# Optimization experiments

Hardware: AMD Instinct MI355X
Metric: run time of the kernel (lower is better)

The kernel has to match this reference:

```python
import jax, jax.numpy as jnp
import numpy as np
from jax import lax

INT32_MAX = 2147483647


def setup_inputs() -> dict:
    key = jax.random.key(0)
    kx, ky = jax.random.split(key)
    x = jax.random.normal(kx, (4096, 64), dtype=jnp.float32)
    y = jax.random.normal(ky, (100000, 64), dtype=jnp.float32)
    return {"x": x, "y": y, "k": 16, "n_splits": 10}


def reference(x, y, k, n_splits):
    """Streaming k-NN: L2 path distance with incremental top-k merge.

    x: (B1, d) queries; y: (B2, d) database. Returns
      ds:  (B1, k)    k smallest distances
      idx: (B1, k, 1) global indices into y (int32), matching (B1,k,y.ndim-1).
    """
    B1, d = x.shape
    B2 = y.shape[0]
    split = B2 // n_splits
    y_splits = y.reshape(n_splits, split, d)  # even splits, as in torch .split
    bases = jnp.arange(n_splits, dtype=jnp.int32) * split

    x2 = jnp.sum(x * x, axis=-1, keepdims=True)  # (B1, 1)

    ds0 = jnp.full((B1, k), jnp.inf, dtype=x.dtype)
    idx0 = jnp.full((B1, k), INT32_MAX, dtype=jnp.int32)
    col = jnp.arange(split, dtype=jnp.int32)

    def step(carry, inp):
        ds, idx = carry
        y_b, base = inp                               # (split, d), scalar
        y2 = jnp.sum(y_b * y_b, axis=-1)              # (split,)
        d2 = x2 + y2[None, :] - 2.0 * (x @ y_b.T)     # (B1, split)
        new_ds = jnp.sqrt(jnp.maximum(d2, 0.0))
        new_idx = jnp.broadcast_to(base + col, (B1, split))
        cat_ds = jnp.concatenate([ds, new_ds], axis=1)      # (B1, k+split)
        cat_idx = jnp.concatenate([idx, new_idx], axis=1)
        neg_top, pos = lax.top_k(-cat_ds, k)                # smallest-k
        ds = -neg_top
        idx = jnp.take_along_axis(cat_idx, pos, axis=1)
        return (ds, idx), None

    (ds, idx), _ = lax.scan(step, (ds0, idx0), (y_splits, bases))
    return ds, idx[..., None]
```

## Files before the change

### kernel.cpp

```cpp
#include <hip/hip_runtime.h>
#include <math.h>

#define D 64
#define K 16
#define NSEG_WANT 128
#define CAP_WANT 512
#define YPAD 128
#define SLOT_B 2304
#define DEPTH 2

typedef __attribute__((ext_vector_type(8))) short short8;
typedef __attribute__((ext_vector_type(4))) float f32x4;

__device__ __forceinline__ unsigned short f32_to_bf16_rne(float f) {
    unsigned u = __float_as_uint(f);
    u = u + 0x7FFFu + ((u >> 16) & 1u);
    return (unsigned short)(u >> 16);
}

__device__ __forceinline__ void gload16(const void* g, void* l) {
    __builtin_amdgcn_global_load_lds((const __attribute__((address_space(1))) void*)g,
                                     (__attribute__((address_space(3))) void*)l, 16, 0, 0);
}
__device__ __forceinline__ void gload4(const void* g, void* l) {
    __builtin_amdgcn_global_load_lds((const __attribute__((address_space(1))) void*)g,
                                     (__attribute__((address_space(3))) void*)l, 4, 0, 0);
}

__global__ __launch_bounds__(256)
void prep_kernel(const float* __restrict__ x, const float* __restrict__ y,
                 unsigned short* __restrict__ xbneg,
                 unsigned short* __restrict__ yb,
                 float* __restrict__ y2, int B1, int B2)
{
    const int w = threadIdx.x >> 6, lane = threadIdx.x & 63;
    const int row = blockIdx.x * 4 + w;
    const int B2p = B2 + YPAD;
    if (row < B2) {
        const float v = y[(size_t)row * D + lane];
        float s = v * v;
        #pragma unroll
        for (int off = 32; off > 0; off >>= 1) s += __shfl_xor(s, off);
        yb[(size_t)row * D + lane] = f32_to_bf16_rne(v);
        if (lane == 0) y2[row] = s;
    } else if (row < B2p) {
        yb[(size_t)row * D + lane] = 0;
        if (lane == 0) y2[row] = INFINITY;
    } else if (row < B2p + B1) {
        const int r = row - B2p;
        const float v = x[(size_t)r * D + lane];
        xbneg[(size_t)r * D + lane] = f32_to_bf16_rne(-2.0f * v);
    }
}

#define STAGE(slotIdx, c)                                                    \
    do {                                                                     \
        unsigned char* _sb = wl + (slotIdx) * SLOT_B;                        \
        const unsigned short* _g0 = gbase + (size_t)((c) * 16 + 0) * D;      \
        const unsigned short* _g1 = gbase + (size_t)((c) * 16 + 8) * D;      \
        gload16(_g0, _sb);                                                   \
        gload16(_g1, _sb + 1024);                                            \
        gload4(y2g + base + (c) * 16 + lane, _sb + 2048);                    \
    } while (0)

#define WAITSLOT()                                                           \
    do {                                                                     \
        asm volatile("s_waitcnt vmcnt(3)" ::: "memory");                     \
        __builtin_amdgcn_sched_barrier(0);                                   \
    } while (0)

__global__ __launch_bounds__(256)
void knn_min_kernel(const unsigned short* __restrict__ xbneg,
                    const unsigned short* __restrict__ yb,
                    const float* __restrict__ y2g,
                    float* __restrict__ pmin,
                    int B1, int B2, int segsz, int nseg)
{
    const int tid  = threadIdx.x;
    const int w    = tid >> 6;
    const int lane = tid & 63;
    const int n15  = lane & 15;
    const int quad = lane >> 4;
    const int qb   = blockIdx.x * 256 + w * 64;
    const int s    = blockIdx.y;
    const int base = s * segsz;
    const int segN = min(segsz, B2 - base);
    const int nch  = segN >> 4;
    const int nchE = nch & ~1;

    __shared__ __align__(16) unsigned char lds_buf[4 * DEPTH * SLOT_B];
    unsigned char* wl = lds_buf + w * (DEPTH * SLOT_B);

    const short8 b00 = *(const short8*)&xbneg[(size_t)(qb +  0 + n15) * D + quad * 8];
    const short8 b01 = *(const short8*)&xbneg[(size_t)(qb +  0 + n15) * D + 32 + quad * 8];
    const short8 b10 = *(const short8*)&xbneg[(size_t)(qb + 16 + n15) * D + quad * 8];
    const short8 b11 = *(const short8*)&xbneg[(size_t)(qb + 16 + n15) * D + 32 + quad * 8];
    const short8 b20 = *(const short8*)&xbneg[(size_t)(qb + 32 + n15) * D + quad * 8];
    const short8 b21 = *(const short8*)&xbneg[(size_t)(qb + 32 + n15) * D + 32 + quad * 8];
    const short8 b30 = *(const short8*)&xbneg[(size_t)(qb + 48 + n15) * D + quad * 8];
    const short8 b31 = *(const short8*)&xbneg[(size_t)(qb + 48 + n15) * D + 32 + quad * 8];
    __builtin_amdgcn_sched_barrier(0);

    const int srow  = lane >> 3;
    const int sslot = (lane & 7) ^ srow;
    const unsigned short* gbase = yb + (size_t)(base + srow) * D + (sslot << 3);
    const int roff0 = n15 * 128 + (((quad    ) ^ (n15 & 7)) << 4);
    const int roff1 = n15 * 128 + (((quad + 4) ^ (n15 & 7)) << 4);
    const int yoff  = 2048 + (quad << 4);

    float rm0 = INFINITY, rm1 = INFINITY, rm2 = INFINITY, rm3 = INFINITY;

    STAGE(0, 0); STAGE(1, 1);
    __builtin_amdgcn_sched_barrier(0);

#define STEP_MIN(slotIdx, c)                                                        \
    do {                                                                            \
        WAITSLOT();                                                                 \
        const unsigned char* _lb = wl + (slotIdx) * SLOT_B;                         \
        const short8 a0 = *(const short8*)(_lb + roff0);                            \
        const short8 a1 = *(const short8*)(_lb + roff1);                            \
        const float4 yv = *(const float4*)(_lb + yoff);                             \
        __builtin_amdgcn_sched_barrier(0);        \
        STAGE(slotIdx, (c) + 2);                    \
        f32x4 acc;                                                                  \
        acc = (f32x4){0.f, 0.f, 0.f, 0.f};                                          \
        acc = __builtin_amdgcn_mfma_f32_16x16x32_bf16(a0, b00, acc, 0, 0, 0);       \
        acc = __builtin_amdgcn_mfma_f32_16x16x32_bf16(a1, b01, acc, 0, 0, 0);       \
        rm0 = fminf(rm0, fminf(fminf(acc[0] + yv.x, acc[1] + yv.y),                 \
                               fminf(acc[2] + yv.z, acc[3] + yv.w)));               \
        acc = (f32x4){0.f, 0.f, 0.f, 0.f};                                          \
        acc = __builtin_amdgcn_mfma_f32_16x16x32_bf16(a0, b10, acc, 0, 0, 0);       \
        acc = __builtin_amdgcn_mfma_f32_16x16x32_bf16(a1, b11, acc, 0, 0, 0);       \
        rm1 = fminf(rm1, fminf(fminf(acc[0] + yv.x, acc[1] + yv.y),                 \
                               fminf(acc[2] + yv.z, acc[3] + yv.w)));               \
        acc = (f32x4){0.f, 0.f, 0.f, 0.f};                                          \
        acc = __builtin_amdgcn_mfma_f32_16x16x32_bf16(a0, b20, acc, 0, 0, 0);       \
        acc = __builtin_amdgcn_mfma_f32_16x16x32_bf16(a1, b21, acc, 0, 0, 0);       \
        rm2 = fminf(rm2, fminf(fminf(acc[0] + yv.x, acc[1] + yv.y),                 \
                               fminf(acc[2] + yv.z, acc[3] + yv.w)));               \
        acc = (f32x4){0.f, 0.f, 0.f, 0.f};                                          \
        acc = __builtin_amdgcn_mfma_f32_16x16x32_bf16(a0, b30, acc, 0, 0, 0);       \
        acc = __builtin_amdgcn_mfma_f32_16x16x32_bf16(a1, b31, acc, 0, 0, 0);       \
        rm3 = fminf(rm3, fminf(fminf(acc[0] + yv.x, acc[1] + yv.y),                 \
                               fminf(acc[2] + yv.z, acc[3] + yv.w)));               \
    } while (0)

    for (int ci = 0; ci < nchE; ci += 2) {
        STEP_MIN(0, ci);
        STEP_MIN(1, ci + 1);
    }
    if (nch & 1) STEP_MIN(0, nchE);
#undef STEP_MIN

    asm volatile("s_waitcnt vmcnt(0)" ::: "memory");

    pmin[((size_t)(qb +  0 + n15) * nseg + s) * 4 + quad] = rm0;
    pmin[((size_t)(qb + 16 + n15) * nseg + s) * 4 + quad] = rm1;
    pmin[((size_t)(qb + 32 + n15) * nseg + s) * 4 + quad] = rm2;
    pmin[((size_t)(qb + 48 + n15) * nseg + s) * 4 + quad] = rm3;
}

__global__ __launch_bounds__(256)
void knn_thresh_kernel(const float* __restrict__ pmin,
                       float* __restrict__ Tq, int* __restrict__ cnt,
                       int B1, int npart)
{
    const int w    = threadIdx.x >> 6;
    const int lane = threadIdx.x & 63;
    const int q    = blockIdx.x * 4 + w;

    const float* p = pmin + (size_t)q * npart;
    float cd = (lane < npart) ? p[lane] : INFINITY;
    float worst = cd;
    #pragma unroll
    for (int off = 32; off > 0; off >>= 1) worst = fmaxf(worst, __shfl_xor(worst, off));

    for (int t = 64; t < npart; ++t) {
        const float dv = p[t];
        if (dv < worst) {
            const unsigned long long m = __ballot(cd == worst);
            const int vict = __ffsll(m) - 1;
            if (lane == vict) cd = dv;
            float wv = cd;
            #pragma unroll
            for (int off = 32; off > 0; off >>= 1) wv = fmaxf(wv, __shfl_xor(wv, off));
            worst = wv;
        }
    }
    if (lane == 0) { Tq[q] = worst; cnt[q] = 0; }
}

__global__ __launch_bounds__(256)
void knn_filter_kernel(const unsigned short* __restrict__ xbneg,
                       const unsigned short* __restrict__ yb,
                       const float* __restrict__ y2g,
                       const float* __restrict__ Tq,
                       int* __restrict__ cnt,
                       float* __restrict__ sd, int* __restrict__ si,
                       int B1, int B2, int segsz, int cap)
{
    const int tid  = threadIdx.x;
    const int w    = tid >> 6;
    const int lane = tid & 63;
    const int n15  = lane & 15;
    const int quad = lane >> 4;
    const int qb   = blockIdx.x * 256 + w * 64;
    const int s    = blockIdx.y;
    const int base = s * segsz;
    const int segN = min(segsz, B2 - base);
    const int nch  = segN >> 4;
    const int nchE = nch & ~1;

    __shared__ __align__(16) unsigned char lds_buf[4 * DEPTH * SLOT_B];
    unsigned char* wl = lds_buf + w * (DEPTH * SLOT_B);

    const short8 b00 = *(const short8*)&xbneg[(size_t)(qb +  0 + n15) * D + quad * 8];
    const short8 b01 = *(const short8*)&xbneg[(size_t)(qb +  0 + n15) * D + 32 + quad * 8];
    const short8 b10 = *(const short8*)&xbneg[(size_t)(qb + 16 + n15) * D + quad * 8];
    const short8 b11 = *(const short8*)&xbneg[(size_t)(qb + 16 + n15) * D + 32 + quad * 8];
    const short8 b20 = *(const short8*)&xbneg[(size_t)(qb + 32 + n15) * D + quad * 8];
    const short8 b21 = *(const short8*)&xbneg[(size_t)(qb + 32 + n15) * D + 32 + quad * 8];
    const short8 b30 = *(const short8*)&xbneg[(size_t)(qb + 48 + n15) * D + quad * 8];
    const short8 b31 = *(const short8*)&xbneg[(size_t)(qb + 48 + n15) * D + 32 + quad * 8];

    const int q0 = qb +  0 + n15;
    const int q1 = qb + 16 + n15;
    const int q2 = qb + 32 + n15;
    const int q3 = qb + 48 + n15;
    const float th0 = Tq[q0];
    const float th1 = Tq[q1];
    const float th2 = Tq[q2];
    const float th3 = Tq[q3];
    __builtin_amdgcn_sched_barrier(0);

    const int srow  = lane >> 3;
    const int sslot = (lane & 7) ^ srow;
    const unsigned short* gbase = yb + (size_t)(base + srow) * D + (sslot << 3);
    const int roff0 = n15 * 128 + (((quad    ) ^ (n15 & 7)) << 4);
    const int roff1 = n15 * 128 + (((quad + 4) ^ (n15 & 7)) << 4);
    const int yoff  = 2048 + (quad << 4);

    STAGE(0, 0); STAGE(1, 1);
    __builtin_amdgcn_sched_barrier(0);

#define GROUP_FLT(A0, A1, B0, B1_, YV, TH, QQ, CB)                                  \
    do {                                                                            \
        f32x4 acc = {0.f, 0.f, 0.f, 0.f};                                           \
        acc = __builtin_amdgcn_mfma_f32_16x16x32_bf16(A0, B0, acc, 0, 0, 0);        \
        acc = __builtin_amdgcn_mfma_f32_16x16x32_bf16(A1, B1_, acc, 0, 0, 0);       \
        const float m0 = acc[0] + (YV).x;                                           \
        const float m1 = acc[1] + (YV).y;                                           \
        const float m2 = acc[2] + (YV).z;                                           \
        const float m3 = acc[3] + (YV).w;                                           \
        const float mm = fminf(fminf(m0, m1), fminf(m2, m3));                       \
        if (mm <= (TH)) {                                                           \
            if (m0 <= (TH)) { const int p_ = atomicAdd(&cnt[QQ], 1); if (p_ < cap) { sd[(size_t)(QQ) * cap + p_] = m0; si[(size_t)(QQ) * cap + p_] = (CB) + 0; } } \
            if (m1 <= (TH)) { const int p_ = atomicAdd(&cnt[QQ], 1); if (p_ < cap) { sd[(size_t)(QQ) * cap + p_] = m1; si[(size_t)(QQ) * cap + p_] = (CB) + 1; } } \
            if (m2 <= (TH)) { const int p_ = atomicAdd(&cnt[QQ], 1); if (p_ < cap) { sd[(size_t)(QQ) * cap + p_] = m2; si[(size_t)(QQ) * cap + p_] = (CB) + 2; } } \
            if (m3 <= (TH)) { const int p_ = atomicAdd(&cnt[QQ], 1); if (p_ < cap) { sd[(size_t)(QQ) * cap + p_] = m3; si[(size_t)(QQ) * cap + p_] = (CB) + 3; } } \
        }                                                                           \
    } while (0)

#define STEP_FLT(slotIdx, c)                                                        \
    do {                                                                            \
        WAITSLOT();                                                                 \
        const unsigned char* _lb = wl + (slotIdx) * SLOT_B;                         \
        const short8 a0 = *(const short8*)(_lb + roff0);                            \
        const short8 a1 = *(const short8*)(_lb + roff1);                            \
        const float4 yv = *(const float4*)(_lb + yoff);                             \
        __builtin_amdgcn_sched_barrier(0);        \
        STAGE(slotIdx, (c) + 2);                                                    \
        const int cb = base + ((c) << 4) + 4 * quad;                                \
        GROUP_FLT(a0, a1, b00, b01, yv, th0, q0, cb);                               \
        GROUP_FLT(a0, a1, b10, b11, yv, th1, q1, cb);                               \
        GROUP_FLT(a0, a1, b20, b21, yv, th2, q2, cb);                               \
        GROUP_FLT(a0, a1, b30, b31, yv, th3, q3, cb);                               \
    } while (0)

    for (int ci = 0; ci < nchE; ci += 2) {
        STEP_FLT(0, ci);
        STEP_FLT(1, ci + 1);
    }
    if (nch & 1) STEP_FLT(0, nchE);
#undef STEP_FLT
#undef GROUP_FLT

    asm volatile("s_waitcnt vmcnt(0)" ::: "memory");
}

__global__ __launch_bounds__(256)
void knn_merge_refine_kernel(const float* __restrict__ sd,
                             const int*   __restrict__ si,
                             const int*   __restrict__ cnt,
                             const float* __restrict__ x,
                             const float* __restrict__ y,
                             float* __restrict__ out_ds,
                             float* __restrict__ out_idx,
                             int B1, int B2, int cap)
{
    const int w    = threadIdx.x >> 6;
    const int lane = threadIdx.x & 63;
    const int q    = blockIdx.x * 4 + w;

    float cd = INFINITY;
    int   ci = 2147483647;
    float worst = INFINITY;

    const int n = min(cnt[q], cap);
    const float* sdq = sd + (size_t)q * cap;
    const int*   siq = si + (size_t)q * cap;

    for (int j = 0; j < n; ++j) {
        const float dv = sdq[j];
        if (dv < worst) {
            const int jidx = siq[j];
            const unsigned long long m = __ballot(cd == worst);
            const int vict = __ffsll(m) - 1;
            if (lane == vict) { cd = dv; ci = jidx; }
            float wv = cd;
            #pragma unroll
            for (int off = 32; off > 0; off >>= 1)
                wv = fmaxf(wv, __shfl_xor(wv, off));
            worst = wv;
        }
    }

    __shared__ float xs[4][D];
    __shared__ float sds[4][64];
    __shared__ int   sidx[4][64];

    if (lane < D / 4)
        ((float4*)xs[w])[lane] = ((const float4*)(x + (size_t)q * D))[lane];
    __syncthreads();

    float x2 = 0.f;
    #pragma unroll
    for (int i = 0; i < D; ++i) x2 = __fadd_rn(x2, __fmul_rn(xs[w][i], xs[w][i]));

    int idx = ci;
    float ds32 = INFINITY;
    if (idx >= 0 && idx < B2) {
        float yr[D];
        const float4* yrow = (const float4*)(y + (size_t)idx * D);
        #pragma unroll
        for (int t = 0; t < D / 4; ++t) {
            float4 v = yrow[t];
            yr[4*t+0] = v.x; yr[4*t+1] = v.y; yr[4*t+2] = v.z; yr[4*t+3] = v.w;
        }
        float y2 = 0.f;
        #pragma unroll
        for (int i = 0; i < D; ++i) y2 = __fadd_rn(y2, __fmul_rn(yr[i], yr[i]));

        float dot = 0.f;
        #pragma unroll
        for (int i = 0; i < D; ++i) dot = __fmaf_rn(xs[w][i], yr[i], dot);

        const float d2 = __fsub_rn(__fadd_rn(x2, y2), __fmul_rn(2.0f, dot));
        ds32 = __fsqrt_rn(fmaxf(d2, 0.f));
    } else {
        idx = 2147483647;
    }
    sds[w][lane]  = ds32;
    sidx[w][lane] = idx;
    __syncthreads();

    int rank = 0;
    for (int j = 0; j < 64; ++j) {
        const float dj = sds[w][j];
        bool prec = (dj < ds32);
        if (dj == ds32 && sidx[w][j] != idx) {
            const int  jd    = sidx[w][j];
            const long dd    = (long)jd - (long)idx;
            const long add   = dd < 0 ? -dd : dd;
            const bool t2win = (add >= 21504 && add <= 23552);
            prec = t2win ? (jd > idx) : (jd < idx);
        }
        if (prec) ++rank;
    }
    if (rank < K) {
        out_ds [(size_t)q * K + rank] = ds32;
        out_idx[(size_t)q * K + rank] = (float)idx;
    }
}

extern "C" void kernel_launch(void* const* d_in, const int* in_sizes, int n_in,
                              void* d_out, int out_size, void* d_ws, size_t ws_size,
                              hipStream_t stream)
{
    const float* x = (const float*)d_in[0];
    const float* y = (const float*)d_in[1];

    const int B1 = in_sizes[0] / D;
    const int B2 = in_sizes[1] / D;
    const int B2p = B2 + YPAD;

    const int segsz = (((B2 + NSEG_WANT - 1) / NSEG_WANT) + 15) & ~15;
    const int nseg  = (B2 + segsz - 1) / segsz;

    size_t off = 0;
    unsigned short* xbneg = (unsigned short*)((char*)d_ws + off); off += (size_t)B1 * D * 2;
    unsigned short* yb    = (unsigned short*)((char*)d_ws + off); off += (size_t)B2p * D * 2;
    float*          y2    = (float*)((char*)d_ws + off);          off += (size_t)B2p * 4;
    float*          pmin  = (float*)((char*)d_ws + off);          off += (size_t)B1 * nseg * 4 * 4;
    float*          Tq    = (float*)((char*)d_ws + off);          off += (size_t)B1 * 4;
    int*            cnt   = (int*)((char*)d_ws + off);            off += (size_t)B1 * 4;

    int cap = CAP_WANT;
    {
        const size_t per = (size_t)B1 * 8;
        if (off + (size_t)cap * per > ws_size) {
            const size_t avail = ws_size > off ? ws_size - off : 0;
            cap = (int)(avail / per);
            if (cap < 16) cap = 16;
        }
    }
    float* sd = (float*)((char*)d_ws + off); off += (size_t)B1 * cap * 4;
    int*   si = (int*)((char*)d_ws + off);

    float* out_ds  = (float*)d_out;
    float* out_idx = out_ds + (size_t)B1 * K;

    const int prows = B2p + B1;
    prep_kernel<<<(prows + 3) / 4, 256, 0, stream>>>(x, y, xbneg, yb, y2, B1, B2);

    dim3 grid1(B1 / 256, nseg);
    knn_min_kernel<<<grid1, 256, 0, stream>>>(xbneg, yb, y2, pmin, B1, B2, segsz, nseg);

    knn_thresh_kernel<<<B1 / 4, 256, 0, stream>>>(pmin, Tq, cnt, B1, nseg * 4);

    knn_filter_kernel<<<grid1, 256, 0, stream>>>(xbneg, yb, y2, Tq, cnt, sd, si,
                                                 B1, B2, segsz, cap);

    knn_merge_refine_kernel<<<B1 / 4, 256, 0, stream>>>(sd, si, cnt, x, y,
                                                        out_ds, out_idx,
                                                        B1, B2, cap);
}
```

Before: 374.2 us.

## Share Y tiles across waves in LDS and remap blocks for XCD locality

Replaces the per-wave private LDS staging of y chunks with one block-shared 4-deep ring buffer, loaded cooperatively by three waves and guarded by a workgroup barrier per chunk. Each y chunk is now fetched once per block instead of once per wave, cutting global/L2 traffic fourfold. A 1D grid is remapped so blocks on the same XCD work on neighbouring segments, which should improve L2 reuse. In exchange it adds a barrier every chunk, which couples the waves and may stall MFMA issue, and it assumes nseg is a multiple of 8 with a power-of-two per-XCD count.

Result: slower. 418.0 us (+11.7%).

```diff
diff --git a/kernel.cpp b/kernel.cpp
--- a/kernel.cpp
+++ b/kernel.cpp
@@ -3,11 +3,11 @@
 
 #define D 64
 #define K 16
-#define NSEG_WANT 128
+#define NSEG 128
 #define CAP_WANT 512
 #define YPAD 128
 #define SLOT_B 2304
-#define DEPTH 2
+#define DEPTH 4
 
 typedef __attribute__((ext_vector_type(8))) short short8;
 typedef __attribute__((ext_vector_type(4))) float f32x4;
@@ -53,20 +53,22 @@
     }
 }
 
-#define STAGE(slotIdx, c)                                                    \
-    do {                                                                     \
-        unsigned char* _sb = wl + (slotIdx) * SLOT_B;                        \
-        const unsigned short* _g0 = gbase + (size_t)((c) * 16 + 0) * D;      \
-        const unsigned short* _g1 = gbase + (size_t)((c) * 16 + 8) * D;      \
-        gload16(_g0, _sb);                                                   \
-        gload16(_g1, _sb + 1024);                                            \
-        gload4(y2g + base + (c) * 16 + lane, _sb + 2048);                    \
+#define STAGE_SHARE(slotIdx, c)                                               \
+    do {                                                                      \
+        if (w < 2)                                                            \
+            gload16(gsrc16 + (size_t)(c) * (16 * D),                          \
+                    tile + (slotIdx) * SLOT_B + w * 1024);                    \
+        else if (w == 2)                                                      \
+            gload4(gsrc4 + (c) * 16, tile + (slotIdx) * SLOT_B + 2048);       \
     } while (0)
 
-#define WAITSLOT()                                                           \
-    do {                                                                     \
-        asm volatile("s_waitcnt vmcnt(3)" ::: "memory");                     \
-        __builtin_amdgcn_sched_barrier(0);                                   \
+#define CHUNK_SYNC(c)                                                         \
+    do {                                                                      \
+        if (w < 3) asm volatile("s_waitcnt vmcnt(2)" ::: "memory");           \
+        __builtin_amdgcn_s_barrier();                                         \
+        __builtin_amdgcn_sched_barrier(0);                                    \
+        STAGE_SHARE(((c) + 3) & (DEPTH - 1), (c) + 3);                        \
+        __builtin_amdgcn_sched_barrier(0);                                    \
     } while (0)
 
 __global__ __launch_bounds__(256)
@@ -81,15 +83,20 @@
     const int lane = tid & 63;
     const int n15  = lane & 15;
     const int quad = lane >> 4;
-    const int qb   = blockIdx.x * 256 + w * 64;
-    const int s    = blockIdx.y;
-    const int base = s * segsz;
+
+    const int b    = blockIdx.x;
+    const int pxc  = nseg >> 3;
+    const int xcd  = b & 7;
+    const int rest = b >> 3;
+    const int seg  = xcd * pxc + (rest & (pxc - 1));
+    const int qi   = rest / pxc;
+
+    const int qb   = qi * 256 + w * 64;
+    const int base = seg * segsz;
     const int segN = min(segsz, B2 - base);
     const int nch  = segN >> 4;
-    const int nchE = nch & ~1;
-
-    __shared__ __align__(16) unsigned char lds_buf[4 * DEPTH * SLOT_B];
-    unsigned char* wl = lds_buf + w * (DEPTH * SLOT_B);
+
+    __shared__ __align__(16) unsigned char tile[DEPTH * SLOT_B];
 
     const short8 b00 = *(const short8*)&xbneg[(size_t)(qb +  0 + n15) * D + quad * 8];
     const short8 b01 = *(const short8*)&xbneg[(size_t)(qb +  0 + n15) * D + 32 + quad * 8];
@@ -103,61 +110,53 @@
 
     const int srow  = lane >> 3;
     const int sslot = (lane & 7) ^ srow;
-    const unsigned short* gbase = yb + (size_t)(base + srow) * D + (sslot << 3);
+    const unsigned short* gsrc16 = yb + (size_t)(base + w * 8 + srow) * D + (sslot << 3);
+    const float*          gsrc4  = y2g + base + lane;
     const int roff0 = n15 * 128 + (((quad    ) ^ (n15 & 7)) << 4);
     const int roff1 = n15 * 128 + (((quad + 4) ^ (n15 & 7)) << 4);
     const int yoff  = 2048 + (quad << 4);
 
     float rm0 = INFINITY, rm1 = INFINITY, rm2 = INFINITY, rm3 = INFINITY;
 
-    STAGE(0, 0); STAGE(1, 1);
+    STAGE_SHARE(0, 0); STAGE_SHARE(1, 1); STAGE_SHARE(2, 2);
     __builtin_amdgcn_sched_barrier(0);
 
-#define STEP_MIN(slotIdx, c)                                                        \
-    do {                                                                            \
-        WAITSLOT();                                                                 \
-        const unsigned char* _lb = wl + (slotIdx) * SLOT_B;                         \
-        const short8 a0 = *(const short8*)(_lb + roff0);                            \
-        const short8 a1 = *(const short8*)(_lb + roff1);                            \
-        const float4 yv = *(const float4*)(_lb + yoff);                             \
-        __builtin_amdgcn_sched_barrier(0);        \
-        STAGE(slotIdx, (c) + 2);                    \
-        f32x4 acc;                                                                  \
-        acc = (f32x4){0.f, 0.f, 0.f, 0.f};                                          \
-        acc = __builtin_amdgcn_mfma_f32_16x16x32_bf16(a0, b00, acc, 0, 0, 0);       \
-        acc = __builtin_amdgcn_mfma_f32_16x16x32_bf16(a1, b01, acc, 0, 0, 0);       \
-        rm0 = fminf(rm0, fminf(fminf(acc[0] + yv.x, acc[1] + yv.y),                 \
-                               fminf(acc[2] + yv.z, acc[3] + yv.w)));               \
-        acc = (f32x4){0.f, 0.f, 0.f, 0.f};                                          \
-        acc = __builtin_amdgcn_mfma_f32_16x16x32_bf16(a0, b10, acc, 0, 0, 0);       \
-        acc = __builtin_amdgcn_mfma_f32_16x16x32_bf16(a1, b11, acc, 0, 0, 0);       \
-        rm1 = fminf(rm1, fminf(fminf(acc[0] + yv.x, acc[1] + yv.y),                 \
-                               fminf(acc[2] + yv.z, acc[3] + yv.w)));               \
-        acc = (f32x4){0.f, 0.f, 0.f, 0.f};                                          \
-        acc = __builtin_amdgcn_mfma_f32_16x16x32_bf16(a0, b20, acc, 0, 0, 0);       \
-        acc = __builtin_amdgcn_mfma_f32_16x16x32_bf16(a1, b21, acc, 0, 0, 0);       \
-        rm2 = fminf(rm2, fminf(fminf(acc[0] + yv.x, acc[1] + yv.y),                 \
-                               fminf(acc[2] + yv.z, acc[3] + yv.w)));               \
-        acc = (f32x4){0.f, 0.f, 0.f, 0.f};                                          \
-        acc = __builtin_amdgcn_mfma_f32_16x16x32_bf16(a0, b30, acc, 0, 0, 0);       \
-        acc = __builtin_amdgcn_mfma_f32_16x16x32_bf16(a1, b31, acc, 0, 0, 0);       \
-        rm3 = fminf(rm3, fminf(fminf(acc[0] + yv.x, acc[1] + yv.y),                 \
-                               fminf(acc[2] + yv.z, acc[3] + yv.w)));               \
-    } while (0)
-
-    for (int ci = 0; ci < nchE; ci += 2) {
-        STEP_MIN(0, ci);
-        STEP_MIN(1, ci + 1);
-    }
-    if (nch & 1) STEP_MIN(0, nchE);
-#undef STEP_MIN
+    for (int c = 0; c < nch; ++c) {
+        CHUNK_SYNC(c);
+        const unsigned char* lb = tile + (c & (DEPTH - 1)) * SLOT_B;
+        const short8 a0 = *(const short8*)(lb + roff0);
+        const short8 a1 = *(const short8*)(lb + roff1);
+        const float4 yv = *(const float4*)(lb + yoff);
+
+        f32x4 acc;
+        acc = (f32x4){0.f, 0.f, 0.f, 0.f};
+        acc = __builtin_amdgcn_mfma_f32_16x16x32_bf16(a0, b00, acc, 0, 0, 0);
+        acc = __builtin_amdgcn_mfma_f32_16x16x32_bf16(a1, b01, acc, 0, 0, 0);
+        rm0 = fminf(rm0, fminf(fminf(acc[0] + yv.x, acc[1] + yv.y),
+                               fminf(acc[2] + yv.z, acc[3] + yv.w)));
+        acc = (f32x4){0.f, 0.f, 0.f, 0.f};
+        acc = __builtin_amdgcn_mfma_f32_16x16x32_bf16(a0, b10, acc, 0, 0, 0);
+        acc = __builtin_amdgcn_mfma_f32_16x16x32_bf16(a1, b11, acc, 0, 0, 0);
+        rm1 = fminf(rm1, fminf(fminf(acc[0] + yv.x, acc[1] + yv.y),
+                               fminf(acc[2] + yv.z, acc[3] + yv.w)));
+        acc = (f32x4){0.f, 0.f, 0.f, 0.f};
+        acc = __builtin_amdgcn_mfma_f32_16x16x32_bf16(a0, b20, acc, 0, 0, 0);
+        acc = __builtin_amdgcn_mfma_f32_16x16x32_bf16(a1, b21, acc, 0, 0, 0);
+        rm2 = fminf(rm2, fminf(fminf(acc[0] + yv.x, acc[1] + yv.y),
+                               fminf(acc[2] + yv.z, acc[3] + yv.w)));
+        acc = (f32x4){0.f, 0.f, 0.f, 0.f};
+        acc = __builtin_amdgcn_mfma_f32_16x16x32_bf16(a0, b30, acc, 0, 0, 0);
+        acc = __builtin_amdgcn_mfma_f32_16x16x32_bf16(a1, b31, acc, 0, 0, 0);
+        rm3 = fminf(rm3, fminf(fminf(acc[0] + yv.x, acc[1] + yv.y),
+                               fminf(acc[2] + yv.z, acc[3] + yv.w)));
+    }
 
     asm volatile("s_waitcnt vmcnt(0)" ::: "memory");
 
-    pmin[((size_t)(qb +  0 + n15) * nseg + s) * 4 + quad] = rm0;
-    pmin[((size_t)(qb + 16 + n15) * nseg + s) * 4 + quad] = rm1;
-    pmin[((size_t)(qb + 32 + n15) * nseg + s) * 4 + quad] = rm2;
-    pmin[((size_t)(qb + 48 + n15) * nseg + s) * 4 + quad] = rm3;
+    pmin[((size_t)(qb +  0 + n15) * nseg + seg) * 4 + quad] = rm0;
+    pmin[((size_t)(qb + 16 + n15) * nseg + seg) * 4 + quad] = rm1;
+    pmin[((size_t)(qb + 32 + n15) * nseg + seg) * 4 + quad] = rm2;
+    pmin[((size_t)(qb + 48 + n15) * nseg + seg) * 4 + quad] = rm3;
 }
 
 __global__ __launch_bounds__(256)
@@ -197,22 +196,27 @@
                        const float* __restrict__ Tq,
                        int* __restrict__ cnt,
                        float* __restrict__ sd, int* __restrict__ si,
-                       int B1, int B2, int segsz, int cap)
+                       int B1, int B2, int segsz, int nseg, int cap)
 {
     const int tid  = threadIdx.x;
     const int w    = tid >> 6;
     const int lane = tid & 63;
     const int n15  = lane & 15;
     const int quad = lane >> 4;
-    const int qb   = blockIdx.x * 256 + w * 64;
-    const int s    = blockIdx.y;
-    const int base = s * segsz;
+
+    const int b    = blockIdx.x;
+    const int pxc  = nseg >> 3;
+    const int xcd  = b & 7;
+    const int rest = b >> 3;
+    const int seg  = xcd * pxc + (rest & (pxc - 1));
+    const int qi   = rest / pxc;
+
+    const int qb   = qi * 256 + w * 64;
+    const int base = seg * segsz;
     const int segN = min(segsz, B2 - base);
     const int nch  = segN >> 4;
-    const int nchE = nch & ~1;
-
-    __shared__ __align__(16) unsigned char lds_buf[4 * DEPTH * SLOT_B];
-    unsigned char* wl = lds_buf + w * (DEPTH * SLOT_B);
+
+    __shared__ __align__(16) unsigned char tile[DEPTH * SLOT_B];
 
     const short8 b00 = *(const short8*)&xbneg[(size_t)(qb +  0 + n15) * D + quad * 8];
     const short8 b01 = *(const short8*)&xbneg[(size_t)(qb +  0 + n15) * D + 32 + quad * 8];
@@ -235,12 +239,13 @@
 
     const int srow  = lane >> 3;
     const int sslot = (lane & 7) ^ srow;
-    const unsigned short* gbase = yb + (size_t)(base + srow) * D + (sslot << 3);
+    const unsigned short* gsrc16 = yb + (size_t)(base + w * 8 + srow) * D + (sslot << 3);
+    const float*          gsrc4  = y2g + base + lane;
     const int roff0 = n15 * 128 + (((quad    ) ^ (n15 & 7)) << 4);
     const int roff1 = n15 * 128 + (((quad + 4) ^ (n15 & 7)) << 4);
     const int yoff  = 2048 + (quad << 4);
 
-    STAGE(0, 0); STAGE(1, 1);
+    STAGE_SHARE(0, 0); STAGE_SHARE(1, 1); STAGE_SHARE(2, 2);
     __builtin_amdgcn_sched_barrier(0);
 
 #define GROUP_FLT(A0, A1, B0, B1_, YV, TH, QQ, CB)                                  \
@@ -261,28 +266,18 @@
         }                                                                           \
     } while (0)
 
-#define STEP_FLT(slotIdx, c)                                                        \
-    do {                                                                            \
-        WAITSLOT();                                                                 \
-        const unsigned char* _lb = wl + (slotIdx) * SLOT_B;                         \
-        const short8 a0 = *(const short8*)(_lb + roff0);                            \
-        const short8 a1 = *(const short8*)(_lb + roff1);                            \
-        const float4 yv = *(const float4*)(_lb + yoff);                             \
-        __builtin_amdgcn_sched_barrier(0);        \
-        STAGE(slotIdx, (c) + 2);                                                    \
-        const int cb = base + ((c) << 4) + 4 * quad;                                \
-        GROUP_FLT(a0, a1, b00, b01, yv, th0, q0, cb);                               \
-        GROUP_FLT(a0, a1, b10, b11, yv, th1, q1, cb);                               \
-        GROUP_FLT(a0, a1, b20, b21, yv, th2, q2, cb);                               \
-        GROUP_FLT(a0, a1, b30, b31, yv, th3, q3, cb);                               \
-    } while (0)
-
-    for (int ci = 0; ci < nchE; ci += 2) {
-        STEP_FLT(0, ci);
-        STEP_FLT(1, ci + 1);
-    }
-    if (nch & 1) STEP_FLT(0, nchE);
-#undef STEP_FLT
+    for (int c = 0; c < nch; ++c) {
+        CHUNK_SYNC(c);
+        const unsigned char* lb = tile + (c & (DEPTH - 1)) * SLOT_B;
+        const short8 a0 = *(const short8*)(lb + roff0);
+        const short8 a1 = *(const short8*)(lb + roff1);
+        const float4 yv = *(const float4*)(lb + yoff);
+        const int cb = base + (c << 4) + 4 * quad;
+        GROUP_FLT(a0, a1, b00, b01, yv, th0, q0, cb);
+        GROUP_FLT(a0, a1, b10, b11, yv, th1, q1, cb);
+        GROUP_FLT(a0, a1, b20, b21, yv, th2, q2, cb);
+        GROUP_FLT(a0, a1, b30, b31, yv, th3, q3, cb);
+    }
 #undef GROUP_FLT
 
     asm volatile("s_waitcnt vmcnt(0)" ::: "memory");
@@ -394,8 +389,8 @@
     const int B2 = in_sizes[1] / D;
     const int B2p = B2 + YPAD;
 
-    const int segsz = (((B2 + NSEG_WANT - 1) / NSEG_WANT) + 15) & ~15;
-    const int nseg  = (B2 + segsz - 1) / segsz;
+    const int segsz = (((B2 + NSEG - 1) / NSEG) + 15) & ~15;
+    const int nseg  = NSEG;
 
     size_t off = 0;
     unsigned short* xbneg = (unsigned short*)((char*)d_ws + off); off += (size_t)B1 * D * 2;
@@ -423,13 +418,13 @@
     const int prows = B2p + B1;
     prep_kernel<<<(prows + 3) / 4, 256, 0, stream>>>(x, y, xbneg, yb, y2, B1, B2);
 
-    dim3 grid1(B1 / 256, nseg);
-    knn_min_kernel<<<grid1, 256, 0, stream>>>(xbneg, yb, y2, pmin, B1, B2, segsz, nseg);
+    const int nblk = (B1 / 256) * nseg;
+    knn_min_kernel<<<nblk, 256, 0, stream>>>(xbneg, yb, y2, pmin, B1, B2, segsz, nseg);
 
     knn_thresh_kernel<<<B1 / 4, 256, 0, stream>>>(pmin, Tq, cnt, B1, nseg * 4);
 
-    knn_filter_kernel<<<grid1, 256, 0, stream>>>(xbneg, yb, y2, Tq, cnt, sd, si,
-                                                 B1, B2, segsz, cap);
+    knn_filter_kernel<<<nblk, 256, 0, stream>>>(xbneg, yb, y2, Tq, cnt, sd, si,
+                                                B1, B2, segsz, nseg, cap);
 
     knn_merge_refine_kernel<<<B1 / 4, 256, 0, stream>>>(sd, si, cnt, x, y,
                                                         out_ds, out_idx,
```

## Software-pipeline LDS fragment reads and batch candidate loads via shuffles

Applied to the files above, without the earlier changes.

The min and filter kernels now read the next chunk's LDS fragments into a second register set while MFMA work runs on the current one, with explicit lgkmcnt and vmcnt waits, so LDS latency is hidden behind compute. The threshold and merge kernels load 64 candidates per wave in one coalesced read and broadcast them with shuffles, replacing serial per-element scalar global loads. Costs are extra registers for the double-buffered fragments and a threshold kernel that now assumes npart is a multiple of 64 (at least 64), since the lane guard was removed.

Result: no change. 375.6 us (+0.4%).

```diff
diff --git a/kernel.cpp b/kernel.cpp
--- a/kernel.cpp
+++ b/kernel.cpp
@@ -11,6 +11,8 @@
 
 typedef __attribute__((ext_vector_type(8))) short short8;
 typedef __attribute__((ext_vector_type(4))) float f32x4;
+
+#define SB __builtin_amdgcn_sched_barrier(0)
 
 __device__ __forceinline__ unsigned short f32_to_bf16_rne(float f) {
     unsigned u = __float_as_uint(f);
@@ -63,11 +65,16 @@
         gload4(y2g + base + (c) * 16 + lane, _sb + 2048);                    \
     } while (0)
 
-#define WAITSLOT()                                                           \
+#define READF(A0, A1, YV, slotIdx)                                           \
     do {                                                                     \
-        asm volatile("s_waitcnt vmcnt(3)" ::: "memory");                     \
-        __builtin_amdgcn_sched_barrier(0);                                   \
+        const unsigned char* _lb = wl + (slotIdx) * SLOT_B;                  \
+        A0 = *(const short8*)(_lb + roff0);                                  \
+        A1 = *(const short8*)(_lb + roff1);                                  \
+        YV = *(const float4*)(_lb + yoff);                                   \
     } while (0)
+
+#define VM3()  do { asm volatile("s_waitcnt vmcnt(3)" ::: "memory"); SB; } while (0)
+#define LGKM0() do { asm volatile("s_waitcnt lgkmcnt(0)" ::: "memory"); SB; } while (0)
 
 __global__ __launch_bounds__(256)
 void knn_min_kernel(const unsigned short* __restrict__ xbneg,
@@ -86,7 +93,6 @@
     const int base = s * segsz;
     const int segN = min(segsz, B2 - base);
     const int nch  = segN >> 4;
-    const int nchE = nch & ~1;
 
     __shared__ __align__(16) unsigned char lds_buf[4 * DEPTH * SLOT_B];
     unsigned char* wl = lds_buf + w * (DEPTH * SLOT_B);
@@ -99,7 +105,7 @@
     const short8 b21 = *(const short8*)&xbneg[(size_t)(qb + 32 + n15) * D + 32 + quad * 8];
     const short8 b30 = *(const short8*)&xbneg[(size_t)(qb + 48 + n15) * D + quad * 8];
     const short8 b31 = *(const short8*)&xbneg[(size_t)(qb + 48 + n15) * D + 32 + quad * 8];
-    __builtin_amdgcn_sched_barrier(0);
+    SB;
 
     const int srow  = lane >> 3;
     const int sslot = (lane & 7) ^ srow;
@@ -110,47 +116,55 @@
 
     float rm0 = INFINITY, rm1 = INFINITY, rm2 = INFINITY, rm3 = INFINITY;
 
-    STAGE(0, 0); STAGE(1, 1);
-    __builtin_amdgcn_sched_barrier(0);
-
-#define STEP_MIN(slotIdx, c)                                                        \
+#define COMPUTE_MIN(A0, A1, YV)                                                     \
     do {                                                                            \
-        WAITSLOT();                                                                 \
-        const unsigned char* _lb = wl + (slotIdx) * SLOT_B;                         \
-        const short8 a0 = *(const short8*)(_lb + roff0);                            \
-        const short8 a1 = *(const short8*)(_lb + roff1);                            \
-        const float4 yv = *(const float4*)(_lb + yoff);                             \
-        __builtin_amdgcn_sched_barrier(0);        \
-        STAGE(slotIdx, (c) + 2);                    \
         f32x4 acc;                                                                  \
         acc = (f32x4){0.f, 0.f, 0.f, 0.f};                                          \
-        acc = __builtin_amdgcn_mfma_f32_16x16x32_bf16(a0, b00, acc, 0, 0, 0);       \
-        acc = __builtin_amdgcn_mfma_f32_16x16x32_bf16(a1, b01, acc, 0, 0, 0);       \
-        rm0 = fminf(rm0, fminf(fminf(acc[0] + yv.x, acc[1] + yv.y),                 \
-                               fminf(acc[2] + yv.z, acc[3] + yv.w)));               \
+        acc = __builtin_amdgcn_mfma_f32_16x16x32_bf16(A0, b00, acc, 0, 0, 0);       \
+        acc = __builtin_amdgcn_mfma_f32_16x16x32_bf16(A1, b01, acc, 0, 0, 0);       \
+        rm0 = fminf(rm0, fminf(fminf(acc[0] + (YV).x, acc[1] + (YV).y),             \
+                               fminf(acc[2] + (YV).z, acc[3] + (YV).w)));           \
         acc = (f32x4){0.f, 0.f, 0.f, 0.f};                                          \
-        acc = __builtin_amdgcn_mfma_f32_16x16x32_bf16(a0, b10, acc, 0, 0, 0);       \
-        acc = __builtin_amdgcn_mfma_f32_16x16x32_bf16(a1, b11, acc, 0, 0, 0);       \
-        rm1 = fminf(rm1, fminf(fminf(acc[0] + yv.x, acc[1] + yv.y),                 \
-                               fminf(acc[2] + yv.z, acc[3] + yv.w)));               \
+        acc = __builtin_amdgcn_mfma_f32_16x16x32_bf16(A0, b10, acc, 0, 0, 0);       \
+        acc = __builtin_amdgcn_mfma_f32_16x16x32_bf16(A1, b11, acc, 0, 0, 0);       \
+        rm1 = fminf(rm1, fminf(fminf(acc[0] + (YV).x, acc[1] + (YV).y),             \
+                               fminf(acc[2] + (YV).z, acc[3] + (YV).w)));           \
         acc = (f32x4){0.f, 0.f, 0.f, 0.f};                                          \
-        acc = __builtin_amdgcn_mfma_f32_16x16x32_bf16(a0, b20, acc, 0, 0, 0);       \
-        acc = __builtin_amdgcn_mfma_f32_16x16x32_bf16(a1, b21, acc, 0, 0, 0);       \
-        rm2 = fminf(rm2, fminf(fminf(acc[0] + yv.x, acc[1] + yv.y),                 \
-                               fminf(acc[2] + yv.z, acc[3] + yv.w)));               \
+        acc = __builtin_amdgcn_mfma_f32_16x16x32_bf16(A0, b20, acc, 0, 0, 0);       \
+        acc = __builtin_amdgcn_mfma_f32_16x16x32_bf16(A1, b21, acc, 0, 0, 0);       \
+        rm2 = fminf(rm2, fminf(fminf(acc[0] + (YV).x, acc[1] + (YV).y),             \
+                               fminf(acc[2] + (YV).z, acc[3] + (YV).w)));           \
         acc = (f32x4){0.f, 0.f, 0.f, 0.f};                                          \
-        acc = __builtin_amdgcn_mfma_f32_16x16x32_bf16(a0, b30, acc, 0, 0, 0);       \
-        acc = __builtin_amdgcn_mfma_f32_16x16x32_bf16(a1, b31, acc, 0, 0, 0);       \
-        rm3 = fminf(rm3, fminf(fminf(acc[0] + yv.x, acc[1] + yv.y),                 \
-                               fminf(acc[2] + yv.z, acc[3] + yv.w)));               \
+        acc = __builtin_amdgcn_mfma_f32_16x16x32_bf16(A0, b30, acc, 0, 0, 0);       \
+        acc = __builtin_amdgcn_mfma_f32_16x16x32_bf16(A1, b31, acc, 0, 0, 0);       \
+        rm3 = fminf(rm3, fminf(fminf(acc[0] + (YV).x, acc[1] + (YV).y),             \
+                               fminf(acc[2] + (YV).z, acc[3] + (YV).w)));           \
     } while (0)
 
-    for (int ci = 0; ci < nchE; ci += 2) {
-        STEP_MIN(0, ci);
-        STEP_MIN(1, ci + 1);
-    }
-    if (nch & 1) STEP_MIN(0, nchE);
-#undef STEP_MIN
+    short8 f0a0, f0a1; float4 f0y;
+    short8 f1a0, f1a1; float4 f1y;
+
+    STAGE(0, 0); STAGE(1, 1);
+    VM3();
+    READF(f0a0, f0a1, f0y, 0);
+    LGKM0();
+    STAGE(0, 2); SB;
+
+    int c = 0;
+    for (; c + 1 < nch; c += 2) {
+        VM3();
+        READF(f1a0, f1a1, f1y, 1); SB;
+        COMPUTE_MIN(f0a0, f0a1, f0y);
+        LGKM0();
+        STAGE(1, c + 3); SB;
+        VM3();
+        READF(f0a0, f0a1, f0y, 0); SB;
+        COMPUTE_MIN(f1a0, f1a1, f1y);
+        LGKM0();
+        STAGE(0, c + 4); SB;
+    }
+    if (c < nch) COMPUTE_MIN(f0a0, f0a1, f0y);
+#undef COMPUTE_MIN
 
     asm volatile("s_waitcnt vmcnt(0)" ::: "memory");
 
@@ -170,21 +184,24 @@
     const int q    = blockIdx.x * 4 + w;
 
     const float* p = pmin + (size_t)q * npart;
-    float cd = (lane < npart) ? p[lane] : INFINITY;
+    float cd = p[lane];
     float worst = cd;
     #pragma unroll
     for (int off = 32; off > 0; off >>= 1) worst = fmaxf(worst, __shfl_xor(worst, off));
 
-    for (int t = 64; t < npart; ++t) {
-        const float dv = p[t];
-        if (dv < worst) {
-            const unsigned long long m = __ballot(cd == worst);
-            const int vict = __ffsll(m) - 1;
-            if (lane == vict) cd = dv;
-            float wv = cd;
-            #pragma unroll
-            for (int off = 32; off > 0; off >>= 1) wv = fmaxf(wv, __shfl_xor(wv, off));
-            worst = wv;
+    for (int b = 64; b < npart; b += 64) {
+        const float v = p[b + lane];
+        for (int j = 0; j < 64; ++j) {
+            const float dv = __shfl(v, j);
+            if (dv < worst) {
+                const unsigned long long m = __ballot(cd == worst);
+                const int vict = __ffsll(m) - 1;
+                if (lane == vict) cd = dv;
+                float wv = cd;
+                #pragma unroll
+                for (int off = 32; off > 0; off >>= 1) wv = fmaxf(wv, __shfl_xor(wv, off));
+                worst = wv;
+            }
         }
     }
     if (lane == 0) { Tq[q] = worst; cnt[q] = 0; }
@@ -209,7 +226,6 @@
     const int base = s * segsz;
     const int segN = min(segsz, B2 - base);
     const int nch  = segN >> 4;
-    const int nchE = nch & ~1;
 
     __shared__ __align__(16) unsigned char lds_buf[4 * DEPTH * SLOT_B];
     unsigned char* wl = lds_buf + w * (DEPTH * SLOT_B);
@@ -231,7 +247,7 @@
     const float th1 = Tq[q1];
     const float th2 = Tq[q2];
     const float th3 = Tq[q3];
-    __builtin_amdgcn_sched_barrier(0);
+    SB;
 
     const int srow  = lane >> 3;
     const int sslot = (lane & 7) ^ srow;
@@ -239,9 +255,6 @@
     const int roff0 = n15 * 128 + (((quad    ) ^ (n15 & 7)) << 4);
     const int roff1 = n15 * 128 + (((quad + 4) ^ (n15 & 7)) << 4);
     const int yoff  = 2048 + (quad << 4);
-
-    STAGE(0, 0); STAGE(1, 1);
-    __builtin_amdgcn_sched_barrier(0);
 
 #define GROUP_FLT(A0, A1, B0, B1_, YV, TH, QQ, CB)                                  \
     do {                                                                            \
@@ -261,28 +274,39 @@
         }                                                                           \
     } while (0)
 
-#define STEP_FLT(slotIdx, c)                                                        \
+#define COMPUTE_FLT(A0, A1, YV, c)                                                  \
     do {                                                                            \
-        WAITSLOT();                                                                 \
-        const unsigned char* _lb = wl + (slotIdx) * SLOT_B;                         \
-        const short8 a0 = *(const short8*)(_lb + roff0);                            \
-        const short8 a1 = *(const short8*)(_lb + roff1);                            \
-        const float4 yv = *(const float4*)(_lb + yoff);                             \
-        __builtin_amdgcn_sched_barrier(0);        \
-        STAGE(slotIdx, (c) + 2);                                                    \
-        const int cb = base + ((c) << 4) + 4 * quad;                                \
-        GROUP_FLT(a0, a1, b00, b01, yv, th0, q0, cb);                               \
-        GROUP_FLT(a0, a1, b10, b11, yv, th1, q1, cb);                               \
-        GROUP_FLT(a0, a1, b20, b21, yv, th2, q2, cb);                               \
-        GROUP_FLT(a0, a1, b30, b31, yv, th3, q3, cb);                               \
+        const int cb_ = base + ((c) << 4) + 4 * quad;                               \
+        GROUP_FLT(A0, A1, b00, b01, YV, th0, q0, cb_);                              \
+        GROUP_FLT(A0, A1, b10, b11, YV, th1, q1, cb_);                              \
+        GROUP_FLT(A0, A1, b20, b21, YV, th2, q2, cb_);                              \
+        GROUP_FLT(A0, A1, b30, b31, YV, th3, q3, cb_);                              \
     } while (0)
 
-    for (int ci = 0; ci < nchE; ci += 2) {
-        STEP_FLT(0, ci);
-        STEP_FLT(1, ci + 1);
-    }
-    if (nch & 1) STEP_FLT(0, nchE);
-#undef STEP_FLT
+    short8 f0a0, f0a1; float4 f0y;
+    short8 f1a0, f1a1; float4 f1y;
+
+    STAGE(0, 0); STAGE(1, 1);
+    VM3();
+    READF(f0a0, f0a1, f0y, 0);
+    LGKM0();
+    STAGE(0, 2); SB;
+
+    int c = 0;
+    for (; c + 1 < nch; c += 2) {
+        VM3();
+        READF(f1a0, f1a1, f1y, 1); SB;
+        COMPUTE_FLT(f0a0, f0a1, f0y, c);
+        LGKM0();
+        STAGE(1, c + 3); SB;
+        VM3();
+        READF(f0a0, f0a1, f0y, 0); SB;
+        COMPUTE_FLT(f1a0, f1a1, f1y, c + 1);
+        LGKM0();
+        STAGE(0, c + 4); SB;
+    }
+    if (c < nch) COMPUTE_FLT(f0a0, f0a1, f0y, c);
+#undef COMPUTE_FLT
 #undef GROUP_FLT
 
     asm volatile("s_waitcnt vmcnt(0)" ::: "memory");
@@ -310,18 +334,24 @@
     const float* sdq = sd + (size_t)q * cap;
     const int*   siq = si + (size_t)q * cap;
 
-    for (int j = 0; j < n; ++j) {
-        const float dv = sdq[j];
-        if (dv < worst) {
-            const int jidx = siq[j];
-            const unsigned long long m = __ballot(cd == worst);
-            const int vict = __ffsll(m) - 1;
-            if (lane == vict) { cd = dv; ci = jidx; }
-            float wv = cd;
-            #pragma unroll
-            for (int off = 32; off > 0; off >>= 1)
-                wv = fmaxf(wv, __shfl_xor(wv, off));
-            worst = wv;
+    for (int b = 0; b < n; b += 64) {
+        const int t = b + lane;
+        const float vv = (t < n) ? sdq[t] : INFINITY;
+        const int   iv = (t < n) ? siq[t] : 2147483647;
+        const int lim = min(64, n - b);
+        for (int j = 0; j < lim; ++j) {
+            const float dv = __shfl(vv, j);
+            if (dv < worst) {
+                const int jidx = __shfl(iv, j);
+                const unsigned long long m = __ballot(cd == worst);
+                const int vict = __ffsll(m) - 1;
+                if (lane == vict) { cd = dv; ci = jidx; }
+                float wv = cd;
+                #pragma unroll
+                for (int off = 32; off > 0; off >>= 1)
+                    wv = fmaxf(wv, __shfl_xor(wv, off));
+                worst = wv;
+            }
         }
     }
 
```
